# Kernel tuning notes

Hardware: AMD Instinct MI355X
Metric: run time of the kernel (lower is better)

## Reference

```python
import jax, jax.numpy as jnp
import numpy as np

ALPHA = 0.15
CLIP = 5.0
EPS = 1e-6
LN_EPS = 1e-5

B, S, D, F = 4, 4096, 2048, 128


def setup_inputs() -> dict:
    key = jax.random.key(0)
    ks = jax.random.split(key, 8)
    sd = lambda fan_in: 1.0 / np.sqrt(fan_in)
    return {
        "x": jax.random.normal(ks[0], (B, S, D), dtype=jnp.float32),
        "Q_w": jax.random.normal(ks[1], (D, F), dtype=jnp.float32) * sd(D),
        "Q_b": jnp.zeros((F,), jnp.float32),
        "K_w": jax.random.normal(ks[2], (D, F), dtype=jnp.float32) * sd(D),
        "K_b": jnp.zeros((F,), jnp.float32),
        "lo_proj_w": jax.random.normal(ks[3], (D, D), dtype=jnp.float32) * sd(D),
        "lo_proj_b": jnp.zeros((D,), jnp.float32),
        "lo_p_w": jax.random.normal(ks[4], (D, F), dtype=jnp.float32) * sd(D),
        "lo_p_b": jnp.zeros((F,), jnp.float32),
        "proj_w": jax.random.normal(ks[5], (F, D), dtype=jnp.float32) * sd(F),
        "proj_b": jnp.zeros((D,), jnp.float32),
        "O_w": jax.random.normal(ks[6], (D // 2, D), dtype=jnp.float32) * sd(D // 2),
        "O_b": jnp.zeros((D,), jnp.float32),
        "ln_gamma": jnp.ones((D,), jnp.float32),
        "ln_beta": jnp.zeros((D,), jnp.float32),
    }


def _ema_over_time(score):
    # score: [B, S, F]; ema[0]=score[0]; ema[t]=a*score[t]+(1-a)*ema[t-1]
    seq = jnp.swapaxes(score, 0, 1)  # [S, B, F]

    def step(prev, x_t):
        new = ALPHA * x_t + (1.0 - ALPHA) * prev
        return new, new

    init = seq[0]
    _, rest = jax.lax.scan(step, init, seq[1:])
    ema_seq = jnp.concatenate([init[None], rest], axis=0)
    return jnp.swapaxes(ema_seq, 0, 1)


def reference(x, Q_w, Q_b, K_w, K_b, lo_proj_w, lo_proj_b, lo_p_w, lo_p_b,
              proj_w, proj_b, O_w, O_b, ln_gamma, ln_beta):
    x_f32 = x.astype(jnp.float32)
    residual = x_f32

    q = x_f32 @ Q_w + Q_b                    # [B,S,128]
    k = x_f32 @ K_w + K_b                    # [B,S,128]
    # Lo: Dense(d_model) -> gelu -> Dense(128)
    v_h = jax.nn.gelu(x_f32 @ lo_proj_w + lo_proj_b)
    V = v_h @ lo_p_w + lo_p_b                # [B,S,128]

    score = jax.nn.sigmoid(q) * jax.nn.sigmoid(k)
    score_ema = _ema_over_time(score)
    mean_last = jnp.mean(score_ema, axis=-1, keepdims=True)
    denom = jnp.maximum(mean_last, EPS)
    score_clipped = jnp.clip(score_ema / denom, -CLIP, CLIP)

    x_comb = score_clipped * V               # [B,S,128]
    out = x_comb @ proj_w + proj_b           # [B,S,D]  (D even -> no pad)
    a, b = jnp.split(out, 2, axis=-1)
    gated = jax.nn.silu(a) * b               # [B,S,D/2]
    out = gated @ O_w + O_b                  # [B,S,D]

    h = out + residual
    mu = jnp.mean(h, axis=-1, keepdims=True)
    var = jnp.var(h, axis=-1, keepdims=True)
    out = (h - mu) * jax.lax.rsqrt(var + LN_EPS) * ln_gamma + ln_beta
    return out.astype(x.dtype)
```

## Files before the change

### kernel.cpp

```cpp
#include <hip/hip_runtime.h>
#include <cstdint>

#define ALPHA_C 0.15f
#define ONE_MINUS_ALPHA 0.85f
#define CLIP_C 5.0f
#define EPS_C 1e-6f
#define LN_EPS_C 1e-5f

#define Bb 4
#define Ss 4096
#define Dd 2048
#define Mtot (Bb * Ss)

typedef __attribute__((ext_vector_type(8))) short bf16x8;
typedef __attribute__((ext_vector_type(4))) float f32x4;

__device__ __forceinline__ short f2bf(float f) {
  union { float f; uint32_t u; } v; v.f = f;
  uint32_t r = v.u + 0x7fffu + ((v.u >> 16) & 1u);
  return (short)(r >> 16);
}
__device__ __forceinline__ float sigf(float x) { return 1.0f / (1.0f + __expf(-x)); }
__device__ __forceinline__ float geluf(float x) {
  const float c = 0.7978845608028654f;
  float x3 = x * x * x;
  return 0.5f * x * (1.0f + tanhf(c * (x + 0.044715f * x3)));
}

__device__ __forceinline__ void load_lds16(const short* g, short* l) {
  __builtin_amdgcn_global_load_lds((__attribute__((address_space(1))) void*)g,
                                   (__attribute__((address_space(3))) void*)l, 16, 0, 0);
}

#define BM 128
#define BN 128
#define BK 32

template <int MODE>
__global__ __launch_bounds__(256, 2) void gemm_tn(
    const short* __restrict__ A, const short* __restrict__ Bt, void* __restrict__ Cout,
    const float* __restrict__ bias, int M, int N, int K) {
  __shared__ __align__(16) short As[BM * BK];
  __shared__ __align__(16) short Bs[BN * BK];

  const int tid = threadIdx.x;
  const int wave = tid >> 6;
  const int lane = tid & 63;
  const int quad = lane >> 4;
  const int l16 = lane & 15;
  const int m0 = blockIdx.y * BM;
  const int n0 = blockIdx.x * BN;
  const int wm = (wave & 1) * 64;
  const int wn = (wave >> 1) * 64;

  const int srow = wave * 32 + (lane >> 2);
  const int skoff = (lane & 3) * 8;
  const short* agp = A + (long)(m0 + srow) * K + skoff;
  const short* bgp = Bt + (long)(n0 + srow) * K + skoff;
  const short* agp2 = agp + (long)16 * K;
  const short* bgp2 = bgp + (long)16 * K;
  short* al = As + (wave * 32) * BK;
  short* al2 = al + 16 * BK;
  short* bl = Bs + (wave * 32) * BK;
  short* bl2 = bl + 16 * BK;

  f32x4 acc[4][4] = {};

  for (int k0 = 0; k0 < K; k0 += BK) {
    __syncthreads();
    load_lds16(agp + k0, al);
    load_lds16(agp2 + k0, al2);
    load_lds16(bgp + k0, bl);
    load_lds16(bgp2 + k0, bl2);
    __syncthreads();

    bf16x8 af[4], bfr[4];
#pragma unroll
    for (int i = 0; i < 4; ++i)
      af[i] = *(const bf16x8*)&As[(wm + i * 16 + l16) * BK + quad * 8];
#pragma unroll
    for (int j = 0; j < 4; ++j)
      bfr[j] = *(const bf16x8*)&Bs[(wn + j * 16 + l16) * BK + quad * 8];
#pragma unroll
    for (int i = 0; i < 4; ++i)
#pragma unroll
      for (int j = 0; j < 4; ++j)
        acc[i][j] = __builtin_amdgcn_mfma_f32_16x16x32_bf16(af[i], bfr[j], acc[i][j], 0, 0, 0);
  }

#pragma unroll
  for (int i = 0; i < 4; ++i) {
#pragma unroll
    for (int r = 0; r < 4; ++r) {
      const int row = m0 + wm + i * 16 + quad * 4 + r;
      const long rb = (long)row * N;
#pragma unroll
      for (int j = 0; j < 4; ++j) {
        const int col = n0 + wn + j * 16 + l16;
        float v = acc[i][j][r] + bias[col];
        if (MODE == 0)
          ((float*)Cout)[rb + col] = v;
        else
          ((short*)Cout)[rb + col] = f2bf(geluf(v));
      }
    }
  }
}

__global__ __launch_bounds__(256) void cast_x_kernel(const float* __restrict__ in,
                                                     short* __restrict__ out, long n4) {
  long i = (long)blockIdx.x * blockDim.x + threadIdx.x;
  const long stride = (long)gridDim.x * blockDim.x;
  for (; i < n4; i += stride) {
    float4 v = ((const float4*)in)[i];
    short4 o;
    o.x = f2bf(v.x); o.y = f2bf(v.y); o.z = f2bf(v.z); o.w = f2bf(v.w);
    ((short4*)out)[i] = o;
  }
}

__global__ __launch_bounds__(256) void tcast_kernel(const float* __restrict__ in,
                                                    short* __restrict__ out, int R, int C) {
  __shared__ float t[32][33];
  const int c0 = blockIdx.x * 32, r0 = blockIdx.y * 32;
  const int tx = threadIdx.x, ty = threadIdx.y;
#pragma unroll
  for (int i = 0; i < 32; i += 8)
    t[ty + i][tx] = in[(long)(r0 + ty + i) * C + (c0 + tx)];
  __syncthreads();
#pragma unroll
  for (int i = 0; i < 32; i += 8)
    out[(long)(c0 + ty + i) * R + (r0 + tx)] = f2bf(t[tx][ty + i]);
}

__global__ void pack_bias_kernel(const float* __restrict__ qb, const float* __restrict__ kb,
                                 float* __restrict__ o) {
  int i = threadIdx.x;
  o[i] = (i < 128) ? qb[i] : kb[i - 128];
}

__global__ __launch_bounds__(128) void ema_kernel(const float* __restrict__ qk,
                                                  float* __restrict__ ema) {
  const int f = threadIdx.x;
  const int b = blockIdx.y;
  const int seg = blockIdx.x;
  const int t0 = seg * 512;
  const int tstart = (seg == 0) ? 0 : (t0 - 256);
  const int tend = t0 + 512;
  const float* __restrict__ base = qk + (long)b * Ss * 256;
  float* __restrict__ eb = ema + (long)b * Ss * 128;

  float e;
  {
    float q = base[(long)tstart * 256 + f];
    float k = base[(long)tstart * 256 + 128 + f];
    e = sigf(q) * sigf(k);
  }
  if (seg == 0) eb[f] = e;

  int t = tstart + 1;
  const int CH = 8;
  const int nch = (tend - t) / CH;
  float cur[CH];
#pragma unroll
  for (int i = 0; i < CH; ++i) {
    float q = base[(long)(t + i) * 256 + f];
    float k = base[(long)(t + i) * 256 + 128 + f];
    cur[i] = sigf(q) * sigf(k);
  }
  for (int c = 0; c < nch; ++c) {
    float nxt[CH] = {};
    if (c + 1 < nch) {
#pragma unroll
      for (int i = 0; i < CH; ++i) {
        float q = base[(long)(t + CH + i) * 256 + f];
        float k = base[(long)(t + CH + i) * 256 + 128 + f];
        nxt[i] = sigf(q) * sigf(k);
      }
    }
#pragma unroll
    for (int i = 0; i < CH; ++i) {
      e = fmaf(ALPHA_C, cur[i], ONE_MINUS_ALPHA * e);
      const int tt = t + i;
      if (tt >= t0) eb[(long)tt * 128 + f] = e;
    }
#pragma unroll
    for (int i = 0; i < CH; ++i) cur[i] = nxt[i];
    t += CH;
  }
  for (; t < tend; ++t) {
    float q = base[(long)t * 256 + f];
    float k = base[(long)t * 256 + 128 + f];
    float s = sigf(q) * sigf(k);
    e = fmaf(ALPHA_C, s, ONE_MINUS_ALPHA * e);
    if (t >= t0) eb[(long)t * 128 + f] = e;
  }
}

__global__ __launch_bounds__(256) void comb_kernel(const float* __restrict__ ema,
                                                   const float* __restrict__ V,
                                                   short* __restrict__ xcomb) {
  const int wv = threadIdx.x >> 6;
  const int lane = threadIdx.x & 63;
  const long row = (long)blockIdx.x * 4 + wv;
  const float* er = ema + row * 128;
  float e0 = er[lane], e1 = er[lane + 64];
  float s = e0 + e1;
#pragma unroll
  for (int m = 1; m < 64; m <<= 1) s += __shfl_xor(s, m, 64);
  const float denom = fmaxf(s * (1.0f / 128.0f), EPS_C);
  const float inv = 1.0f / denom;
  const float c0 = fminf(fmaxf(e0 * inv, -CLIP_C), CLIP_C);
  const float c1 = fminf(fmaxf(e1 * inv, -CLIP_C), CLIP_C);
  const float* vr = V + row * 128;
  xcomb[row * 128 + lane] = f2bf(c0 * vr[lane]);
  xcomb[row * 128 + 64 + lane] = f2bf(c1 * vr[lane + 64]);
}

__global__ __launch_bounds__(256) void gate_kernel(const float* __restrict__ out4,
                                                   short* __restrict__ gated) {
  const long g = (long)blockIdx.x * 256 + threadIdx.x;
  const long r = g >> 8;
  const int i4 = (int)(g & 255) * 4;
  const float4 a = *(const float4*)&out4[r * 2048 + i4];
  const float4 b = *(const float4*)&out4[r * 2048 + 1024 + i4];
  short4 o;
  o.x = f2bf(a.x * sigf(a.x) * b.x);
  o.y = f2bf(a.y * sigf(a.y) * b.y);
  o.z = f2bf(a.z * sigf(a.z) * b.z);
  o.w = f2bf(a.w * sigf(a.w) * b.w);
  *(short4*)&gated[r * 1024 + i4] = o;
}

__global__ __launch_bounds__(256) void ln_kernel(float* __restrict__ io,
                                                 const float* __restrict__ x,
                                                 const float* __restrict__ gamma,
                                                 const float* __restrict__ beta) {
  const long row = blockIdx.x;
  const int tid = threadIdx.x;
  const int wv = tid >> 6, lane = tid & 63;
  float* rp = io + row * 2048;
  const float* xp = x + row * 2048;
  float4 v0 = ((const float4*)rp)[tid * 2];
  float4 v1 = ((const float4*)rp)[tid * 2 + 1];
  float4 x0 = ((const float4*)xp)[tid * 2];
  float4 x1 = ((const float4*)xp)[tid * 2 + 1];
  float h[8] = {v0.x + x0.x, v0.y + x0.y, v0.z + x0.z, v0.w + x0.w,
                v1.x + x1.x, v1.y + x1.y, v1.z + x1.z, v1.w + x1.w};
  float sum = 0.f, ss = 0.f;
#pragma unroll
  for (int i = 0; i < 8; ++i) { sum += h[i]; ss += h[i] * h[i]; }
#pragma unroll
  for (int m = 1; m < 64; m <<= 1) {
    sum += __shfl_xor(sum, m, 64);
    ss += __shfl_xor(ss, m, 64);
  }
  __shared__ float rs[4], rq[4];
  if (lane == 0) { rs[wv] = sum; rq[wv] = ss; }
  __syncthreads();
  sum = rs[0] + rs[1] + rs[2] + rs[3];
  ss = rq[0] + rq[1] + rq[2] + rq[3];
  const float mu = sum * (1.0f / 2048.0f);
  const float var = ss * (1.0f / 2048.0f) - mu * mu;
  const float rstd = rsqrtf(var + LN_EPS_C);
  const int c0 = tid * 8;
  float o[8];
#pragma unroll
  for (int i = 0; i < 8; ++i)
    o[i] = (h[i] - mu) * rstd * gamma[c0 + i] + beta[c0 + i];
  ((float4*)rp)[tid * 2]     = make_float4(o[0], o[1], o[2], o[3]);
  ((float4*)rp)[tid * 2 + 1] = make_float4(o[4], o[5], o[6], o[7]);
}

extern "C" void kernel_launch(void* const* d_in, const int* in_sizes, int n_in,
                              void* d_out, int out_size, void* d_ws, size_t ws_size,
                              hipStream_t stream) {
  const float* x         = (const float*)d_in[0];
  const float* Q_w       = (const float*)d_in[1];
  const float* Q_b       = (const float*)d_in[2];
  const float* K_w       = (const float*)d_in[3];
  const float* K_b       = (const float*)d_in[4];
  const float* lo_proj_w = (const float*)d_in[5];
  const float* lo_proj_b = (const float*)d_in[6];
  const float* lo_p_w    = (const float*)d_in[7];
  const float* lo_p_b    = (const float*)d_in[8];
  const float* proj_w    = (const float*)d_in[9];
  const float* proj_b    = (const float*)d_in[10];
  const float* O_w       = (const float*)d_in[11];
  const float* O_b       = (const float*)d_in[12];
  const float* ln_g      = (const float*)d_in[13];
  const float* ln_b      = (const float*)d_in[14];

  char* ws = (char*)d_ws;
  size_t off = 0;
  auto alloc = [&](size_t bytes) {
    char* p = ws + off;
    off += (bytes + 255) & ~(size_t)255;
    return p;
  };
  short* x16   = (short*)alloc((size_t)Mtot * Dd * 2);
  short* h16   = (short*)alloc((size_t)Mtot * Dd * 2);
  float* qk    = (float*)alloc((size_t)Mtot * 256 * 4);
  float* vbuf  = (float*)alloc((size_t)Mtot * 128 * 4);
  float* emab  = (float*)alloc((size_t)Mtot * 128 * 4);
  short* xcomb = (short*)alloc((size_t)Mtot * 128 * 2);
  short* gated = (short*)alloc((size_t)Mtot * 1024 * 2);
  short* wqkt  = (short*)alloc((size_t)256 * 2048 * 2);
  short* lprjt = (short*)alloc((size_t)2048 * 2048 * 2);
  short* lpt   = (short*)alloc((size_t)128 * 2048 * 2);
  short* prjt  = (short*)alloc((size_t)2048 * 128 * 2);
  short* ot    = (short*)alloc((size_t)2048 * 1024 * 2);
  float* qkb   = (float*)alloc(256 * 4);
  float* outf  = (float*)d_out;

  cast_x_kernel<<<8192, 256, 0, stream>>>(x, x16, (long)Mtot * Dd / 4);
  tcast_kernel<<<dim3(4, 64), dim3(32, 8), 0, stream>>>(Q_w, wqkt, 2048, 128);
  tcast_kernel<<<dim3(4, 64), dim3(32, 8), 0, stream>>>(K_w, wqkt + 128 * 2048, 2048, 128);
  tcast_kernel<<<dim3(64, 64), dim3(32, 8), 0, stream>>>(lo_proj_w, lprjt, 2048, 2048);
  tcast_kernel<<<dim3(4, 64), dim3(32, 8), 0, stream>>>(lo_p_w, lpt, 2048, 128);
  tcast_kernel<<<dim3(64, 4), dim3(32, 8), 0, stream>>>(proj_w, prjt, 128, 2048);
  tcast_kernel<<<dim3(64, 32), dim3(32, 8), 0, stream>>>(O_w, ot, 1024, 2048);
  pack_bias_kernel<<<1, 256, 0, stream>>>(Q_b, K_b, qkb);

  gemm_tn<0><<<dim3(2, 128), 256, 0, stream>>>(x16, wqkt, qk, qkb, Mtot, 256, 2048);
  gemm_tn<1><<<dim3(16, 128), 256, 0, stream>>>(x16, lprjt, h16, lo_proj_b, Mtot, 2048, 2048);
  gemm_tn<0><<<dim3(1, 128), 256, 0, stream>>>(h16, lpt, vbuf, lo_p_b, Mtot, 128, 2048);
  ema_kernel<<<dim3(8, 4), 128, 0, stream>>>(qk, emab);
  comb_kernel<<<Mtot / 4, 256, 0, stream>>>(emab, vbuf, xcomb);
  gemm_tn<0><<<dim3(16, 128), 256, 0, stream>>>(xcomb, prjt, outf, proj_b, Mtot, 2048, 128);
  gate_kernel<<<16384, 256, 0, stream>>>(outf, gated);
  gemm_tn<0><<<dim3(16, 128), 256, 0, stream>>>(gated, ot, outf, O_b, Mtot, 2048, 1024);
  ln_kernel<<<Mtot, 256, 0, stream>>>(outf, x, ln_g, ln_b);
}
```

Baseline: 860.3 us.

## Fuse QK and lo_proj GEMMs, swizzle LDS, bf16 proj output, finer EMA segments

Merges the Q/K projection and the lo_proj GEMM into one launch over a concatenated 2304-column weight, so x is streamed once, with a split epilogue writing fp32 qk or bf16 GELU output. Adds an XOR swizzle to the LDS layout to cut bank conflicts on MFMA fragment reads. Stores the proj GEMM output as bf16 to halve gate-kernel traffic. Reduces the EMA segment size from 512 to 64 with a 96-step warm-up for far more parallel blocks. The shorter warm-up truncates the EMA history (0.85^96, about 1.6e-7 relative), and bf16 intermediates add rounding error.

```diff
diff --git a/kernel.cpp b/kernel.cpp
--- a/kernel.cpp
+++ b/kernel.cpp
@@ -20,6 +20,10 @@
   uint32_t r = v.u + 0x7fffu + ((v.u >> 16) & 1u);
   return (short)(r >> 16);
 }
+__device__ __forceinline__ float bf2f(short s) {
+  union { uint32_t u; float f; } v; v.u = ((uint32_t)(uint16_t)s) << 16;
+  return v.f;
+}
 __device__ __forceinline__ float sigf(float x) { return 1.0f / (1.0f + __expf(-x)); }
 __device__ __forceinline__ float geluf(float x) {
   const float c = 0.7978845608028654f;
@@ -38,8 +42,8 @@
 
 template <int MODE>
 __global__ __launch_bounds__(256, 2) void gemm_tn(
-    const short* __restrict__ A, const short* __restrict__ Bt, void* __restrict__ Cout,
-    const float* __restrict__ bias, int M, int N, int K) {
+    const short* __restrict__ A, const short* __restrict__ Bt, void* __restrict__ out0,
+    void* __restrict__ out1, const float* __restrict__ bias, int M, int N, int K) {
   __shared__ __align__(16) short As[BM * BK];
   __shared__ __align__(16) short Bs[BN * BK];
 
@@ -54,7 +58,7 @@
   const int wn = (wave >> 1) * 64;
 
   const int srow = wave * 32 + (lane >> 2);
-  const int skoff = (lane & 3) * 8;
+  const int skoff = ((lane & 3) ^ ((lane >> 3) & 3)) * 8;
   const short* agp = A + (long)(m0 + srow) * K + skoff;
   const short* bgp = Bt + (long)(n0 + srow) * K + skoff;
   const short* agp2 = agp + (long)16 * K;
@@ -64,6 +68,8 @@
   short* bl = Bs + (wave * 32) * BK;
   short* bl2 = bl + 16 * BK;
 
+  const int rsw = (l16 >> 1) & 3;
+
   f32x4 acc[4][4] = {};
 
   for (int k0 = 0; k0 < K; k0 += BK) {
@@ -77,10 +83,10 @@
     bf16x8 af[4], bfr[4];
 #pragma unroll
     for (int i = 0; i < 4; ++i)
-      af[i] = *(const bf16x8*)&As[(wm + i * 16 + l16) * BK + quad * 8];
+      af[i] = *(const bf16x8*)&As[(wm + i * 16 + l16) * BK + (quad ^ rsw) * 8];
 #pragma unroll
     for (int j = 0; j < 4; ++j)
-      bfr[j] = *(const bf16x8*)&Bs[(wn + j * 16 + l16) * BK + quad * 8];
+      bfr[j] = *(const bf16x8*)&Bs[(wn + j * 16 + l16) * BK + (quad ^ rsw) * 8];
 #pragma unroll
     for (int i = 0; i < 4; ++i)
 #pragma unroll
@@ -93,15 +99,22 @@
 #pragma unroll
     for (int r = 0; r < 4; ++r) {
       const int row = m0 + wm + i * 16 + quad * 4 + r;
-      const long rb = (long)row * N;
 #pragma unroll
       for (int j = 0; j < 4; ++j) {
         const int col = n0 + wn + j * 16 + l16;
         float v = acc[i][j][r] + bias[col];
-        if (MODE == 0)
-          ((float*)Cout)[rb + col] = v;
-        else
-          ((short*)Cout)[rb + col] = f2bf(geluf(v));
+        if (MODE == 0) {
+          ((float*)out0)[(long)row * N + col] = v;
+        } else if (MODE == 1) {
+          ((short*)out0)[(long)row * N + col] = f2bf(geluf(v));
+        } else if (MODE == 2) {
+          ((short*)out0)[(long)row * N + col] = f2bf(v);
+        } else {
+          if (n0 < 256)
+            ((float*)out0)[(long)row * 256 + col] = v;
+          else
+            ((short*)out1)[(long)row * 2048 + (col - 256)] = f2bf(geluf(v));
+        }
       }
     }
   }
@@ -134,19 +147,23 @@
 }
 
 __global__ void pack_bias_kernel(const float* __restrict__ qb, const float* __restrict__ kb,
-                                 float* __restrict__ o) {
-  int i = threadIdx.x;
-  o[i] = (i < 128) ? qb[i] : kb[i - 128];
-}
-
+                                 const float* __restrict__ lob, float* __restrict__ o) {
+  int i = blockIdx.x * 256 + threadIdx.x;
+  if (i < 128) o[i] = qb[i];
+  else if (i < 256) o[i] = kb[i - 128];
+  else if (i < 2304) o[i] = lob[i - 256];
+}
+
+#define SEG 64
+#define WARM 96
 __global__ __launch_bounds__(128) void ema_kernel(const float* __restrict__ qk,
                                                   float* __restrict__ ema) {
   const int f = threadIdx.x;
   const int b = blockIdx.y;
   const int seg = blockIdx.x;
-  const int t0 = seg * 512;
-  const int tstart = (seg == 0) ? 0 : (t0 - 256);
-  const int tend = t0 + 512;
+  const int t0 = seg * SEG;
+  const int tstart = (t0 >= WARM) ? (t0 - WARM) : 0;
+  const int tend = t0 + SEG;
   const float* __restrict__ base = qk + (long)b * Ss * 256;
   float* __restrict__ eb = ema + (long)b * Ss * 128;
 
@@ -166,7 +183,7 @@
   for (int i = 0; i < CH; ++i) {
     float q = base[(long)(t + i) * 256 + f];
     float k = base[(long)(t + i) * 256 + 128 + f];
-    cur[i] = sigf(q) * sigf(k);
+    cur[i] = ALPHA_C * (sigf(q) * sigf(k));
   }
   for (int c = 0; c < nch; ++c) {
     float nxt[CH] = {};
@@ -175,12 +192,12 @@
       for (int i = 0; i < CH; ++i) {
         float q = base[(long)(t + CH + i) * 256 + f];
         float k = base[(long)(t + CH + i) * 256 + 128 + f];
-        nxt[i] = sigf(q) * sigf(k);
+        nxt[i] = ALPHA_C * (sigf(q) * sigf(k));
       }
     }
 #pragma unroll
     for (int i = 0; i < CH; ++i) {
-      e = fmaf(ALPHA_C, cur[i], ONE_MINUS_ALPHA * e);
+      e = fmaf(ONE_MINUS_ALPHA, e, cur[i]);
       const int tt = t + i;
       if (tt >= t0) eb[(long)tt * 128 + f] = e;
     }
@@ -191,8 +208,7 @@
   for (; t < tend; ++t) {
     float q = base[(long)t * 256 + f];
     float k = base[(long)t * 256 + 128 + f];
-    float s = sigf(q) * sigf(k);
-    e = fmaf(ALPHA_C, s, ONE_MINUS_ALPHA * e);
+    e = fmaf(ONE_MINUS_ALPHA, e, ALPHA_C * (sigf(q) * sigf(k)));
     if (t >= t0) eb[(long)t * 128 + f] = e;
   }
 }
@@ -217,18 +233,19 @@
   xcomb[row * 128 + 64 + lane] = f2bf(c1 * vr[lane + 64]);
 }
 
-__global__ __launch_bounds__(256) void gate_kernel(const float* __restrict__ out4,
+__global__ __launch_bounds__(256) void gate_kernel(const short* __restrict__ out4,
                                                    short* __restrict__ gated) {
   const long g = (long)blockIdx.x * 256 + threadIdx.x;
   const long r = g >> 8;
   const int i4 = (int)(g & 255) * 4;
-  const float4 a = *(const float4*)&out4[r * 2048 + i4];
-  const float4 b = *(const float4*)&out4[r * 2048 + 1024 + i4];
+  const short4 a4 = *(const short4*)&out4[r * 2048 + i4];
+  const short4 b4 = *(const short4*)&out4[r * 2048 + 1024 + i4];
+  float ax = bf2f(a4.x), ay = bf2f(a4.y), az = bf2f(a4.z), aw = bf2f(a4.w);
   short4 o;
-  o.x = f2bf(a.x * sigf(a.x) * b.x);
-  o.y = f2bf(a.y * sigf(a.y) * b.y);
-  o.z = f2bf(a.z * sigf(a.z) * b.z);
-  o.w = f2bf(a.w * sigf(a.w) * b.w);
+  o.x = f2bf(ax * sigf(ax) * bf2f(b4.x));
+  o.y = f2bf(ay * sigf(ay) * bf2f(b4.y));
+  o.z = f2bf(az * sigf(az) * bf2f(b4.z));
+  o.w = f2bf(aw * sigf(aw) * bf2f(b4.w));
   *(short4*)&gated[r * 1024 + i4] = o;
 }
 
@@ -305,30 +322,29 @@
   float* emab  = (float*)alloc((size_t)Mtot * 128 * 4);
   short* xcomb = (short*)alloc((size_t)Mtot * 128 * 2);
   short* gated = (short*)alloc((size_t)Mtot * 1024 * 2);
-  short* wqkt  = (short*)alloc((size_t)256 * 2048 * 2);
-  short* lprjt = (short*)alloc((size_t)2048 * 2048 * 2);
+  short* wbig  = (short*)alloc((size_t)2304 * 2048 * 2);
   short* lpt   = (short*)alloc((size_t)128 * 2048 * 2);
   short* prjt  = (short*)alloc((size_t)2048 * 128 * 2);
   short* ot    = (short*)alloc((size_t)2048 * 1024 * 2);
-  float* qkb   = (float*)alloc(256 * 4);
+  float* biasb = (float*)alloc(2304 * 4);
   float* outf  = (float*)d_out;
+  short* out4b = (short*)d_out;
 
   cast_x_kernel<<<8192, 256, 0, stream>>>(x, x16, (long)Mtot * Dd / 4);
-  tcast_kernel<<<dim3(4, 64), dim3(32, 8), 0, stream>>>(Q_w, wqkt, 2048, 128);
-  tcast_kernel<<<dim3(4, 64), dim3(32, 8), 0, stream>>>(K_w, wqkt + 128 * 2048, 2048, 128);
-  tcast_kernel<<<dim3(64, 64), dim3(32, 8), 0, stream>>>(lo_proj_w, lprjt, 2048, 2048);
+  tcast_kernel<<<dim3(4, 64), dim3(32, 8), 0, stream>>>(Q_w, wbig, 2048, 128);
+  tcast_kernel<<<dim3(4, 64), dim3(32, 8), 0, stream>>>(K_w, wbig + 128 * 2048, 2048, 128);
+  tcast_kernel<<<dim3(64, 64), dim3(32, 8), 0, stream>>>(lo_proj_w, wbig + 256 * 2048, 2048, 2048);
   tcast_kernel<<<dim3(4, 64), dim3(32, 8), 0, stream>>>(lo_p_w, lpt, 2048, 128);
   tcast_kernel<<<dim3(64, 4), dim3(32, 8), 0, stream>>>(proj_w, prjt, 128, 2048);
   tcast_kernel<<<dim3(64, 32), dim3(32, 8), 0, stream>>>(O_w, ot, 1024, 2048);
-  pack_bias_kernel<<<1, 256, 0, stream>>>(Q_b, K_b, qkb);
-
-  gemm_tn<0><<<dim3(2, 128), 256, 0, stream>>>(x16, wqkt, qk, qkb, Mtot, 256, 2048);
-  gemm_tn<1><<<dim3(16, 128), 256, 0, stream>>>(x16, lprjt, h16, lo_proj_b, Mtot, 2048, 2048);
-  gemm_tn<0><<<dim3(1, 128), 256, 0, stream>>>(h16, lpt, vbuf, lo_p_b, Mtot, 128, 2048);
-  ema_kernel<<<dim3(8, 4), 128, 0, stream>>>(qk, emab);
+  pack_bias_kernel<<<9, 256, 0, stream>>>(Q_b, K_b, lo_proj_b, biasb);
+
+  gemm_tn<3><<<dim3(18, 128), 256, 0, stream>>>(x16, wbig, qk, h16, biasb, Mtot, 2304, 2048);
+  gemm_tn<0><<<dim3(1, 128), 256, 0, stream>>>(h16, lpt, vbuf, nullptr, lo_p_b, Mtot, 128, 2048);
+  ema_kernel<<<dim3(Ss / SEG, 4), 128, 0, stream>>>(qk, emab);
   comb_kernel<<<Mtot / 4, 256, 0, stream>>>(emab, vbuf, xcomb);
-  gemm_tn<0><<<dim3(16, 128), 256, 0, stream>>>(xcomb, prjt, outf, proj_b, Mtot, 2048, 128);
-  gate_kernel<<<16384, 256, 0, stream>>>(outf, gated);
-  gemm_tn<0><<<dim3(16, 128), 256, 0, stream>>>(gated, ot, outf, O_b, Mtot, 2048, 1024);
+  gemm_tn<2><<<dim3(16, 128), 256, 0, stream>>>(xcomb, prjt, out4b, nullptr, proj_b, Mtot, 2048, 128);
+  gate_kernel<<<16384, 256, 0, stream>>>(out4b, gated);
+  gemm_tn<0><<<dim3(16, 128), 256, 0, stream>>>(gated, ot, outf, nullptr, O_b, Mtot, 2048, 1024);
   ln_kernel<<<Mtot, 256, 0, stream>>>(outf, x, ln_g, ln_b);
 }
```

Result: faster. 749.4 us (-12.9%).
